# Performance work log

Measured on AMD Instinct MI355X. Metric: run time of the kernel, lower is better.

Reference implementation:

```python
import jax, jax.numpy as jnp
import numpy as np

PATCH = 15  # box-filter kernel size (odd -> SAME padding == padding=PATCH//2, stride 1)


def _box_filter(x, k):
    """All-ones kxk conv2d, stride 1, zero pad k//2. x: (N,1,H,W).
    The ones kernel is separable: ones(k,k) = ones(k,1) @ ones(1,k)."""
    dn = ('NCHW', 'OIHW', 'NCHW')
    kh = jnp.ones((1, 1, k, 1), x.dtype)
    kw = jnp.ones((1, 1, 1, k), x.dtype)
    x = jax.lax.conv_general_dilated(x, kh, (1, 1), 'SAME', dimension_numbers=dn)
    x = jax.lax.conv_general_dilated(x, kw, (1, 1), 'SAME', dimension_numbers=dn)
    return x


def _rgb_to_yuv420(rgb):
    """rgb: (N,3,H,W) -> y:(N,H,W), u,v:(N,H/2,W/2) (2x2 avg-pooled chroma)."""
    r, g, b = rgb[:, 0], rgb[:, 1], rgb[:, 2]
    y = 0.299 * r + 0.587 * g + 0.114 * b
    u = -0.169 * r - 0.331 * g + 0.5 * b + 128.0
    v = 0.5 * r - 0.46 * g - 0.04 * b + 128.0
    n, h, w = u.shape
    u = u.reshape(n, h // 2, 2, w // 2, 2).mean(axis=(2, 4))
    v = v.reshape(n, h // 2, 2, w // 2, 2).mean(axis=(2, 4))
    return y, u, v


def _filtered_channels(img, k):
    y, u, v = _rgb_to_yuv420(img)
    return (_box_filter(y[:, None], k),
            _box_filter(u[:, None], k),
            _box_filter(v[:, None], k))


def setup_inputs() -> dict:
    key = jax.random.key(0)
    k1, k2 = jax.random.split(key)
    input_ = jax.random.uniform(k1, (16, 3, 512, 512), dtype=jnp.float32)
    target = jax.random.uniform(k2, (16, 3, 512, 512), dtype=jnp.float32)
    return {"input": input_, "target": target}


def reference(input, target):
    yi, ui, vi = _filtered_channels(input, PATCH)
    yt, ut, vt = _filtered_channels(target, PATCH)
    mse = lambda a, b: jnp.mean((a - b) ** 2)
    return mse(yi, yt) + mse(ui, ut) + mse(vi, vt)
```

## Files before the change

kernel.cpp:

```cpp
#include <hip/hip_runtime.h>

#define NIMG 16
#define H 512
#define W 512


static __device__ __forceinline__ void barln() {
    asm volatile("s_waitcnt lgkmcnt(0)" ::: "memory");
    __builtin_amdgcn_s_barrier();
    __builtin_amdgcn_sched_barrier(0);
}

#define ISSUE(px, s0,s1,s2,s3,s4,s5) do { if (doLd) {                        \
    const int yy_ = 2*(px) + rr;                                             \
    const int yc_ = yy_ < 0 ? 0 : (yy_ > H-1 ? H-1 : yy_);                   \
    const size_t off_ = (size_t)yc_ * W + xcl;                               \
    s0 = *(const float4*)(pi + off_);                                        \
    s1 = *(const float4*)(pi + plane + off_);                                \
    s2 = *(const float4*)(pi + 2*plane + off_);                              \
    s3 = *(const float4*)(pt + off_);                                        \
    s4 = *(const float4*)(pt + plane + off_);                                \
    s5 = *(const float4*)(pt + 2*plane + off_);                              \
} } while(0)

#define STAGE(px, s0,s1,s2,s3,s4,s5) do { if (doLd) {                        \
    const int yy_ = 2*(px) + rr;                                             \
    const float m_ = (cOK && (unsigned)yy_ < (unsigned)H) ? 1.f : 0.f;       \
    const int nb_ = (px) & 1;                                                \
    float4 dR_, dG_, dB_, y4_;                                               \
    dR_.x=(s0.x-s3.x)*m_; dR_.y=(s0.y-s3.y)*m_; dR_.z=(s0.z-s3.z)*m_; dR_.w=(s0.w-s3.w)*m_; \
    dG_.x=(s1.x-s4.x)*m_; dG_.y=(s1.y-s4.y)*m_; dG_.z=(s1.z-s4.z)*m_; dG_.w=(s1.w-s4.w)*m_; \
    dB_.x=(s2.x-s5.x)*m_; dB_.y=(s2.y-s5.y)*m_; dB_.z=(s2.z-s5.z)*m_; dB_.w=(s2.w-s5.w)*m_; \
    y4_.x = 0.299f*dR_.x + 0.587f*dG_.x + 0.114f*dB_.x;                      \
    y4_.y = 0.299f*dR_.y + 0.587f*dG_.y + 0.114f*dB_.y;                      \
    y4_.z = 0.299f*dR_.z + 0.587f*dG_.z + 0.114f*dB_.z;                      \
    y4_.w = 0.299f*dR_.w + 0.587f*dG_.w + 0.114f*dB_.w;                      \
    *(float4*)&dYb[nb_][rr][qq << 2] = y4_;                                  \
    const float rA_ = dR_.x+dR_.y, gA_ = dG_.x+dG_.y, bA_ = dB_.x+dB_.y;     \
    const float rB_ = dR_.z+dR_.w, gB_ = dG_.z+dG_.w, bB_ = dB_.z+dB_.w;     \
    *(float2*)&hUVb[nb_][rr][0][qq << 1] =                                   \
        make_float2(-0.169f*rA_ - 0.331f*gA_ + 0.5f*bA_,                     \
                    -0.169f*rB_ - 0.331f*gB_ + 0.5f*bB_);                    \
    *(float2*)&hUVb[nb_][rr][1][qq << 1] =                                   \
        make_float2( 0.5f*rA_ - 0.46f*gA_ - 0.04f*bA_,                       \
                     0.5f*rB_ - 0.46f*gB_ - 0.04f*bB_);                      \
} } while(0)

#define COMPUTE(px) do {                                                     \
    const int cb_ = (px) & 1;                                                \
    if (tid < 128) {                                                         \
        const float* r0_ = dYb[cb_][0];                                      \
        const float* r1_ = dYb[cb_][1];                                      \
        float hb0_ = 0.f, hb1_ = 0.f;                                        \
        _Pragma("unroll")                                                    \
        for (int j_ = 0; j_ < 15; ++j_) {                                    \
            hb0_ += r0_[tid + 9 + j_]; hb1_ += r1_[tid + 9 + j_];            \
        }                                                                    \
        const float rdA_ = ringY[(2*(px)+1) & 15][tid];                      \
        const float rdB_ = ringY[(2*(px)+2) & 15][tid];                      \
        svY += hb0_ - rdA_;                                                  \
        const int y0_ = 2*(px) - 7 - R0;                                     \
        if ((unsigned)y0_ < 64u) accY += svY * svY;                          \
        svY += hb1_ - rdB_;                                                  \
        if ((unsigned)(y0_ + 1) < 64u) accY += svY * svY;                    \
        ringY[(2*(px)) & 15][tid]     = hb0_;                                \
        ringY[(2*(px)+1) & 15][tid]   = hb1_;                                \
    } else {                                                                 \
        const int pl_ = (tid >> 6) & 1;                                      \
        const int cc_ = tid & 63;                                            \
        const float* h0_ = hUVb[cb_][0][pl_];                                \
        const float* h1_ = hUVb[cb_][1][pl_];                                \
        float hbC_ = 0.f;                                                    \
        _Pragma("unroll")                                                    \
        for (int j_ = 0; j_ < 15; ++j_)                                      \
            hbC_ += h0_[cc_ + 1 + j_] + h1_[cc_ + 1 + j_];                   \
        hbC_ *= 0.25f;                                                       \
        float (*rg_)[64] = pl_ ? ringV : ringU;                              \
        svC += hbC_ - rg_[((px)+1) & 15][cc_];                               \
        if ((unsigned)((px) - 7 - P0) < 32u) accC += svC * svC;              \
        rg_[(px) & 15][cc_] = hbC_;                                          \
    }                                                                        \
} while(0)

__global__ __launch_bounds__(256, 2) void fused_stream_kernel(
        const float* __restrict__ in, const float* __restrict__ tgt,
        float invY, float invC, float* __restrict__ partials) {
    __shared__ float dYb[2][2][160];
    __shared__ float hUVb[2][2][2][80];
    __shared__ float ringY[16][128];
    __shared__ float ringU[16][64];
    __shared__ float ringV[16][64];
    __shared__ float part[4];

    const int tid = threadIdx.x;
    const int b = blockIdx.x;
    const int n     = b >> 5;
    const int band  = (b >> 2) & 7;
    const int quart = b & 3;
    const int R0 = band << 6;
    const int C0 = quart << 7;
    const int P0 = band << 5;

    const size_t plane = (size_t)H * W;
    const float* pi = in  + (size_t)n * 3 * plane;
    const float* pt = tgt + (size_t)n * 3 * plane;

    const bool doLd = tid < 80;
    const int rr = tid >= 40 ? 1 : 0;
    const int qq = tid - 40 * rr;
    const int xx = C0 - 16 + (qq << 2);
    const bool cOK = (unsigned)xx < (unsigned)W;
    const int xcl = cOK ? xx : 0;

    for (int i = tid; i < 16 * 128; i += 256) (&ringY[0][0])[i] = 0.f;
    for (int i = tid; i < 16 * 64; i += 256) {
        (&ringU[0][0])[i] = 0.f; (&ringV[0][0])[i] = 0.f;
    }

    float4 o0, o1, o2, o3, o4, o5;
    float4 e0, e1, e2, e3, e4, e5;
    float svY = 0.f, svC = 0.f, accY = 0.f, accC = 0.f;

    const int pS = P0 - 7;
    const int pE = P0 + 38;

    ISSUE(pS, o0, o1, o2, o3, o4, o5);
    STAGE(pS, o0, o1, o2, o3, o4, o5);
    ISSUE(pS + 1, e0, e1, e2, e3, e4, e5);

#pragma unroll 1
    for (int p = pS; p <= pE; p += 2) {
        barln();
        if (p + 2 <= pE) ISSUE(p + 2, o0, o1, o2, o3, o4, o5);
        COMPUTE(p);
        STAGE(p + 1, e0, e1, e2, e3, e4, e5);
        barln();
        if (p + 3 <= pE) ISSUE(p + 3, e0, e1, e2, e3, e4, e5);
        COMPUTE(p + 1);
        if (p + 2 <= pE) STAGE(p + 2, o0, o1, o2, o3, o4, o5);
    }

    float v = accY * invY + accC * invC;
    for (int o = 32; o > 0; o >>= 1) v += __shfl_down(v, o, 64);
    const int lane = tid & 63, wv = tid >> 6;
    if (lane == 0) part[wv] = v;
    __syncthreads();
    if (tid == 0)
        partials[b] = (part[0] + part[1]) + (part[2] + part[3]);
}

__global__ void final_reduce_kernel(const float* __restrict__ partials, int n,
                                    float* __restrict__ out) {
    float s = 0.f;
    for (int i = threadIdx.x; i < n; i += 256) s += partials[i];
    for (int o = 32; o > 0; o >>= 1) s += __shfl_down(s, o, 64);
    __shared__ float part[4];
    const int lane = threadIdx.x & 63, wid = threadIdx.x >> 6;
    if (lane == 0) part[wid] = s;
    __syncthreads();
    if (threadIdx.x == 0)
        *out = part[0] + part[1] + part[2] + part[3];
}

extern "C" void kernel_launch(void* const* d_in, const int* in_sizes, int n_in,
                              void* d_out, int out_size, void* d_ws, size_t ws_size,
                              hipStream_t stream) {
    const float* input  = (const float*)d_in[0];
    const float* target = (const float*)d_in[1];
    float* out = (float*)d_out;
    float* partials = (float*)d_ws;

    const float invY = 1.0f / (float)((size_t)NIMG * H * W);
    const float invC = 1.0f / (float)((size_t)NIMG * (H/2) * (W/2));

    fused_stream_kernel<<<512, 256, 0, stream>>>(input, target, invY, invC, partials);
    final_reduce_kernel<<<1, 256, 0, stream>>>(partials, 512, out);
}
```

Baseline: 147.1 us.

## Rewrite fused kernel as full-row blocks with wave-scan horizontal box sums

Replaces the 128-column tile kernel with 512-thread blocks that each own a full image row width over a 32-row band, computing horizontal 15-wide box sums through wavefront prefix scans (shfl_up) plus small shared-memory halo exchange between waves. Chroma 2x2 pooling is done with a lane-pair xor shuffle, and loads become scalar per-thread coalesced reads of two rows. This removes the halo over-read of column tiles and the redundant 15-tap LDS summation. In exchange it adds shuffle-heavy scans and a barrier per step, uses fewer blocks (256) with larger rings, and the prefix-sum differencing may change float rounding.

```diff
diff --git a/kernel.cpp b/kernel.cpp
--- a/kernel.cpp
+++ b/kernel.cpp
@@ -3,7 +3,6 @@
 #define NIMG 16
 #define H 512
 #define W 512
-
 
 static __device__ __forceinline__ void barln() {
     asm volatile("s_waitcnt lgkmcnt(0)" ::: "memory");
@@ -11,142 +10,156 @@
     __builtin_amdgcn_sched_barrier(0);
 }
 
-#define ISSUE(px, s0,s1,s2,s3,s4,s5) do { if (doLd) {                        \
-    const int yy_ = 2*(px) + rr;                                             \
-    const int yc_ = yy_ < 0 ? 0 : (yy_ > H-1 ? H-1 : yy_);                   \
-    const size_t off_ = (size_t)yc_ * W + xcl;                               \
-    s0 = *(const float4*)(pi + off_);                                        \
-    s1 = *(const float4*)(pi + plane + off_);                                \
-    s2 = *(const float4*)(pi + 2*plane + off_);                              \
-    s3 = *(const float4*)(pt + off_);                                        \
-    s4 = *(const float4*)(pt + plane + off_);                                \
-    s5 = *(const float4*)(pt + 2*plane + off_);                              \
-} } while(0)
+#define ISSUE(p, A0,A1,A2,A3,A4,A5,A6,A7,A8,A9,A10,A11) do {                 \
+    const int ya_ = 2*(p);                                                   \
+    const int yb_ = ya_ + 1;                                                 \
+    const int yca_ = ya_ < 0 ? 0 : (ya_ > H-1 ? H-1 : ya_);                  \
+    const int ycb_ = yb_ < 0 ? 0 : (yb_ > H-1 ? H-1 : yb_);                  \
+    const size_t oa_ = (size_t)yca_ * W + x;                                 \
+    const size_t ob_ = (size_t)ycb_ * W + x;                                 \
+    A0 = pi[oa_];  A1 = pi[plane+oa_];  A2 = pi[2*plane+oa_];                \
+    A3 = pt[oa_];  A4 = pt[plane+oa_];  A5 = pt[2*plane+oa_];                \
+    A6 = pi[ob_];  A7 = pi[plane+ob_];  A8 = pi[2*plane+ob_];                \
+    A9 = pt[ob_];  A10= pt[plane+ob_];  A11= pt[2*plane+ob_];                \
+} while (0)
 
-#define STAGE(px, s0,s1,s2,s3,s4,s5) do { if (doLd) {                        \
-    const int yy_ = 2*(px) + rr;                                             \
-    const float m_ = (cOK && (unsigned)yy_ < (unsigned)H) ? 1.f : 0.f;       \
-    const int nb_ = (px) & 1;                                                \
-    float4 dR_, dG_, dB_, y4_;                                               \
-    dR_.x=(s0.x-s3.x)*m_; dR_.y=(s0.y-s3.y)*m_; dR_.z=(s0.z-s3.z)*m_; dR_.w=(s0.w-s3.w)*m_; \
-    dG_.x=(s1.x-s4.x)*m_; dG_.y=(s1.y-s4.y)*m_; dG_.z=(s1.z-s4.z)*m_; dG_.w=(s1.w-s4.w)*m_; \
-    dB_.x=(s2.x-s5.x)*m_; dB_.y=(s2.y-s5.y)*m_; dB_.z=(s2.z-s5.z)*m_; dB_.w=(s2.w-s5.w)*m_; \
-    y4_.x = 0.299f*dR_.x + 0.587f*dG_.x + 0.114f*dB_.x;                      \
-    y4_.y = 0.299f*dR_.y + 0.587f*dG_.y + 0.114f*dB_.y;                      \
-    y4_.z = 0.299f*dR_.z + 0.587f*dG_.z + 0.114f*dB_.z;                      \
-    y4_.w = 0.299f*dR_.w + 0.587f*dG_.w + 0.114f*dB_.w;                      \
-    *(float4*)&dYb[nb_][rr][qq << 2] = y4_;                                  \
-    const float rA_ = dR_.x+dR_.y, gA_ = dG_.x+dG_.y, bA_ = dB_.x+dB_.y;     \
-    const float rB_ = dR_.z+dR_.w, gB_ = dG_.z+dG_.w, bB_ = dB_.z+dB_.w;     \
-    *(float2*)&hUVb[nb_][rr][0][qq << 1] =                                   \
-        make_float2(-0.169f*rA_ - 0.331f*gA_ + 0.5f*bA_,                     \
-                    -0.169f*rB_ - 0.331f*gB_ + 0.5f*bB_);                    \
-    *(float2*)&hUVb[nb_][rr][1][qq << 1] =                                   \
-        make_float2( 0.5f*rA_ - 0.46f*gA_ - 0.04f*bA_,                       \
-                     0.5f*rB_ - 0.46f*gB_ - 0.04f*bB_);                      \
-} } while(0)
-
-#define COMPUTE(px) do {                                                     \
-    const int cb_ = (px) & 1;                                                \
-    if (tid < 128) {                                                         \
-        const float* r0_ = dYb[cb_][0];                                      \
-        const float* r1_ = dYb[cb_][1];                                      \
-        float hb0_ = 0.f, hb1_ = 0.f;                                        \
-        _Pragma("unroll")                                                    \
-        for (int j_ = 0; j_ < 15; ++j_) {                                    \
-            hb0_ += r0_[tid + 9 + j_]; hb1_ += r1_[tid + 9 + j_];            \
-        }                                                                    \
-        const float rdA_ = ringY[(2*(px)+1) & 15][tid];                      \
-        const float rdB_ = ringY[(2*(px)+2) & 15][tid];                      \
-        svY += hb0_ - rdA_;                                                  \
-        const int y0_ = 2*(px) - 7 - R0;                                     \
-        if ((unsigned)y0_ < 64u) accY += svY * svY;                          \
-        svY += hb1_ - rdB_;                                                  \
-        if ((unsigned)(y0_ + 1) < 64u) accY += svY * svY;                    \
-        ringY[(2*(px)) & 15][tid]     = hb0_;                                \
-        ringY[(2*(px)+1) & 15][tid]   = hb1_;                                \
-    } else {                                                                 \
-        const int pl_ = (tid >> 6) & 1;                                      \
-        const int cc_ = tid & 63;                                            \
-        const float* h0_ = hUVb[cb_][0][pl_];                                \
-        const float* h1_ = hUVb[cb_][1][pl_];                                \
-        float hbC_ = 0.f;                                                    \
-        _Pragma("unroll")                                                    \
-        for (int j_ = 0; j_ < 15; ++j_)                                      \
-            hbC_ += h0_[cc_ + 1 + j_] + h1_[cc_ + 1 + j_];                   \
-        hbC_ *= 0.25f;                                                       \
-        float (*rg_)[64] = pl_ ? ringV : ringU;                              \
-        svC += hbC_ - rg_[((px)+1) & 15][cc_];                               \
-        if ((unsigned)((px) - 7 - P0) < 32u) accC += svC * svC;              \
-        rg_[(px) & 15][cc_] = hbC_;                                          \
-    }                                                                        \
-} while(0)
-
-__global__ __launch_bounds__(256, 2) void fused_stream_kernel(
+__global__ __launch_bounds__(512, 2) void fused_row_kernel(
         const float* __restrict__ in, const float* __restrict__ tgt,
         float invY, float invC, float* __restrict__ partials) {
-    __shared__ float dYb[2][2][160];
-    __shared__ float hUVb[2][2][2][80];
-    __shared__ float ringY[16][128];
-    __shared__ float ringU[16][64];
-    __shared__ float ringV[16][64];
-    __shared__ float part[4];
+    __shared__ float ringY[16][512];
+    __shared__ float ringC[16][512];
+    __shared__ float LP[2][10][2][8];
+    __shared__ float LS[2][10][2][8];
+    __shared__ float CP[2][10][16];
+    __shared__ float CS[2][10][16];
+    __shared__ float part[8];
 
     const int tid = threadIdx.x;
-    const int b = blockIdx.x;
-    const int n     = b >> 5;
-    const int band  = (b >> 2) & 7;
-    const int quart = b & 3;
-    const int R0 = band << 6;
-    const int C0 = quart << 7;
-    const int P0 = band << 5;
+    const int idx  = (blockIdx.x & 7) * 32 + (blockIdx.x >> 3);
+    const int n    = idx >> 4;
+    const int band = idx & 15;
+    const int R0 = band << 5;
+    const int P0 = band << 4;
 
     const size_t plane = (size_t)H * W;
     const float* pi = in  + (size_t)n * 3 * plane;
     const float* pt = tgt + (size_t)n * 3 * plane;
 
-    const bool doLd = tid < 80;
-    const int rr = tid >= 40 ? 1 : 0;
-    const int qq = tid - 40 * rr;
-    const int xx = C0 - 16 + (qq << 2);
-    const bool cOK = (unsigned)xx < (unsigned)W;
-    const int xcl = cOK ? xx : 0;
+    const int x = tid;
+    const int w = tid >> 6;
+    const int l = tid & 63;
 
-    for (int i = tid; i < 16 * 128; i += 256) (&ringY[0][0])[i] = 0.f;
-    for (int i = tid; i < 16 * 64; i += 256) {
-        (&ringU[0][0])[i] = 0.f; (&ringV[0][0])[i] = 0.f;
+    const bool ev = (l & 1) == 0;
+    const float kr = ev ? -0.169f : 0.5f;
+    const float kg = ev ? -0.331f : -0.46f;
+    const float kb = ev ? 0.5f    : -0.04f;
+
+    for (int i = tid; i < 16 * 512; i += 512) {
+        (&ringY[0][0])[i] = 0.f;
+        (&ringC[0][0])[i] = 0.f;
     }
+    if (tid < 320) {
+        (&LP[0][0][0][0])[tid] = 0.f;
+        (&LS[0][0][0][0])[tid] = 0.f;
+        (&CP[0][0][0])[tid] = 0.f;
+        (&CS[0][0][0])[tid] = 0.f;
+    }
+    __syncthreads();
 
-    float4 o0, o1, o2, o3, o4, o5;
-    float4 e0, e1, e2, e3, e4, e5;
     float svY = 0.f, svC = 0.f, accY = 0.f, accC = 0.f;
 
-    const int pS = P0 - 7;
-    const int pE = P0 + 38;
+    auto STEP = [&](int p, int sp,
+                    float v0, float v1, float v2, float v3, float v4, float v5,
+                    float v6, float v7, float v8, float v9, float v10, float v11) {
+        const float ma = ((unsigned)(2 * p)     < (unsigned)H) ? 1.f : 0.f;
+        const float mb = ((unsigned)(2 * p + 1) < (unsigned)H) ? 1.f : 0.f;
+        const float dra = (v0 - v3) * ma, dga = (v1 - v4)  * ma, dba = (v2 - v5)  * ma;
+        const float drb = (v6 - v9) * mb, dgb = (v7 - v10) * mb, dbb = (v8 - v11) * mb;
+        float Q0 = 0.299f * dra + 0.587f * dga + 0.114f * dba;
+        float Q1 = 0.299f * drb + 0.587f * dgb + 0.114f * dbb;
+        const float hr = dra + drb, hg = dga + dgb, hb2 = dba + dbb;
+        const float sr = hr  + __shfl_xor(hr, 1, 64);
+        const float sg = hg  + __shfl_xor(hg, 1, 64);
+        const float sb = hb2 + __shfl_xor(hb2, 1, 64);
+        float Qc = (kr * sr + kg * sg + kb * sb) * 0.25f;
 
-    ISSUE(pS, o0, o1, o2, o3, o4, o5);
-    STAGE(pS, o0, o1, o2, o3, o4, o5);
-    ISSUE(pS + 1, e0, e1, e2, e3, e4, e5);
+#pragma unroll
+        for (int d = 1; d <= 32; d <<= 1) {
+            const float t0 = __shfl_up(Q0, d, 64);
+            const float t1 = __shfl_up(Q1, d, 64);
+            if (l >= d) { Q0 += t0; Q1 += t1; }
+        }
+#pragma unroll
+        for (int d = 2; d <= 32; d <<= 1) {
+            const float tc = __shfl_up(Qc, d, 64);
+            if (l >= d) Qc += tc;
+        }
+        const float T0 = __shfl(Q0, 63, 64);
+        const float T1 = __shfl(Q1, 63, 64);
+        const float Tc = __shfl(Qc, 62 + (l & 1), 64);
+
+        if (l < 7) {
+            LP[sp][w + 1][0][l] = Q0;  LP[sp][w + 1][1][l] = Q1;
+        } else if (l >= 56 && l < 63) {
+            LS[sp][w + 1][0][l - 56] = T0 - Q0;
+            LS[sp][w + 1][1][l - 56] = T1 - Q1;
+        }
+        if (l < 14)                  CP[sp][w + 1][l]      = Qc;
+        else if (l >= 48 && l < 62)  CS[sp][w + 1][l - 48] = Tc - Qc;
+
+        barln();
+
+        const float d70 = __shfl_down(Q0, 7, 64);
+        const float d71 = __shfl_down(Q1, 7, 64);
+        const float u80 = __shfl_up(Q0, 8, 64);
+        const float u81 = __shfl_up(Q1, 8, 64);
+        float h0 = ((l <= 56) ? d70 : T0) - ((l >= 8) ? u80 : 0.f);
+        float h1 = ((l <= 56) ? d71 : T1) - ((l >= 8) ? u81 : 0.f);
+        if (l < 7)   { h0 += LS[sp][w][0][l];        h1 += LS[sp][w][1][l]; }
+        if (l >= 57) { h0 += LP[sp][w + 2][0][l - 57]; h1 += LP[sp][w + 2][1][l - 57]; }
+        const float dc = __shfl_down(Qc, 14, 64);
+        const float uc = __shfl_up(Qc, 16, 64);
+        float hc = ((l <= 49) ? dc : Tc) - ((l >= 16) ? uc : 0.f);
+        if (l < 14)  hc += CS[sp][w][l];
+        if (l >= 50) hc += CP[sp][w + 2][l - 50];
+
+        const int ra = 2 * p, rb = ra + 1;
+        svY += h0 - ringY[(ra + 1) & 15][x];
+        { const int o = ra - 7; if ((unsigned)(o - R0) < 32u) accY += svY * svY; }
+        svY += h1 - ringY[(ra + 2) & 15][x];
+        { const int o = rb - 7; if ((unsigned)(o - R0) < 32u) accY += svY * svY; }
+        ringY[ra & 15][x] = h0;
+        ringY[rb & 15][x] = h1;
+        svC += hc - ringC[(p + 1) & 15][x];
+        { const int oc = p - 7; if ((unsigned)(oc - P0) < 16u) accC += svC * svC; }
+        ringC[p & 15][x] = hc;
+    };
+
+    const int p0 = P0 - 7;
+    float A0,A1,A2,A3,A4,A5,A6,A7,A8,A9,A10,A11;
+    float B0,B1,B2,B3,B4,B5,B6,B7,B8,B9,B10,B11;
+    ISSUE(p0, A0,A1,A2,A3,A4,A5,A6,A7,A8,A9,A10,A11);
 
 #pragma unroll 1
-    for (int p = pS; p <= pE; p += 2) {
-        barln();
-        if (p + 2 <= pE) ISSUE(p + 2, o0, o1, o2, o3, o4, o5);
-        COMPUTE(p);
-        STAGE(p + 1, e0, e1, e2, e3, e4, e5);
-        barln();
-        if (p + 3 <= pE) ISSUE(p + 3, e0, e1, e2, e3, e4, e5);
-        COMPUTE(p + 1);
-        if (p + 2 <= pE) STAGE(p + 2, o0, o1, o2, o3, o4, o5);
+    for (int it = 0; it < 15; ++it) {
+        const int p = p0 + 2 * it;
+        ISSUE(p + 1, B0,B1,B2,B3,B4,B5,B6,B7,B8,B9,B10,B11);
+        STEP(p, 0, A0,A1,A2,A3,A4,A5,A6,A7,A8,A9,A10,A11);
+        if (it < 14)
+            ISSUE(p + 2, A0,A1,A2,A3,A4,A5,A6,A7,A8,A9,A10,A11);
+        STEP(p + 1, 1, B0,B1,B2,B3,B4,B5,B6,B7,B8,B9,B10,B11);
     }
 
     float v = accY * invY + accC * invC;
     for (int o = 32; o > 0; o >>= 1) v += __shfl_down(v, o, 64);
-    const int lane = tid & 63, wv = tid >> 6;
-    if (lane == 0) part[wv] = v;
+    if (l == 0) part[w] = v;
     __syncthreads();
-    if (tid == 0)
-        partials[b] = (part[0] + part[1]) + (part[2] + part[3]);
+    if (tid == 0) {
+        float s = 0.f;
+#pragma unroll
+        for (int j = 0; j < 8; ++j) s += part[j];
+        partials[blockIdx.x] = s;
+    }
 }
 
 __global__ void final_reduce_kernel(const float* __restrict__ partials, int n,
@@ -173,6 +186,6 @@
     const float invY = 1.0f / (float)((size_t)NIMG * H * W);
     const float invC = 1.0f / (float)((size_t)NIMG * (H/2) * (W/2));
 
-    fused_stream_kernel<<<512, 256, 0, stream>>>(input, target, invY, invC, partials);
-    final_reduce_kernel<<<1, 256, 0, stream>>>(partials, 512, out);
+    fused_row_kernel<<<256, 512, 0, stream>>>(input, target, invY, invC, partials);
+    final_reduce_kernel<<<1, 256, 0, stream>>>(partials, 256, out);
 }
```

New measurement: 142.0 us. -3.5%, faster.
